# Kernel tuning notes

Measured on AMD Instinct MI355X. Metric: run time of the kernel, lower is better.

Reference implementation:

```python
import jax, jax.numpy as jnp
import numpy as np

D = 1024
H = 16
HD = 64  # head dim (bert_dim // num_heads, fixed to 64 by module)
EPS = 1e-12


def setup_inputs() -> dict:
    key = jax.random.key(0)
    ks = jax.random.split(key, 12)
    B, S1, S2 = 8, 512, 512
    scale = 0.02
    return {
        "s1_input_tensor": jax.random.normal(ks[0], (B, S1, D), jnp.float32),
        "s2_input_tensor": jax.random.normal(ks[1], (B, S2, D), jnp.float32),
        "s2_attention_mask": jnp.zeros((B, 1, 1, S2), jnp.float32),
        "Wq": jax.random.normal(ks[2], (D, D), jnp.float32) * scale,
        "bq": jnp.zeros((D,), jnp.float32),
        "Wk": jax.random.normal(ks[3], (D, D), jnp.float32) * scale,
        "bk": jnp.zeros((D,), jnp.float32),
        "Wv": jax.random.normal(ks[4], (D, D), jnp.float32) * scale,
        "bv": jnp.zeros((D,), jnp.float32),
        "Wo": jax.random.normal(ks[5], (D, D), jnp.float32) * scale,
        "bo": jnp.zeros((D,), jnp.float32),
        "ln_w": jnp.ones((D,), jnp.float32),
        "ln_b": jnp.zeros((D,), jnp.float32),
        "cl_att": 1,
    }


def _split_heads(x):
    B, S, _ = x.shape
    return x.reshape(B, S, H, HD).transpose(0, 2, 1, 3)  # [B,H,S,HD]


def _layernorm(x, w, b):
    u = jnp.mean(x, axis=-1, keepdims=True)
    s = jnp.mean(jnp.square(x - u), axis=-1, keepdims=True)
    return w * ((x - u) / jnp.sqrt(s + EPS)) + b


def reference(s1_input_tensor, s2_input_tensor, s2_attention_mask,
              Wq, bq, Wk, bk, Wv, bv, Wo, bo, ln_w, ln_b, cl_att):
    # QKV projections (dropout layers act as identity in eval)
    q = _split_heads(s1_input_tensor @ Wq + bq)   # [B,H,S1,HD]
    k = _split_heads(s2_input_tensor @ Wk + bk)   # [B,H,S2,HD]
    v = _split_heads(s2_input_tensor @ Wv + bv)   # [B,H,S2,HD]

    scores = jnp.einsum("bhqd,bhkd->bhqk", q, k) / jnp.sqrt(jnp.float32(HD))
    scores = scores + s2_attention_mask           # broadcast [B,1,1,S2]
    probs = jax.nn.softmax(scores, axis=-1)
    if cl_att:  # static Python flag: second, inverted softmax pass
        probs = jax.nn.softmax(1.0 - probs + s2_attention_mask, axis=-1)

    ctx = jnp.einsum("bhqk,bhkd->bhqd", probs, v)  # [B,H,S1,HD]
    B, _, S1, _ = ctx.shape
    ctx = ctx.transpose(0, 2, 1, 3).reshape(B, S1, D)

    # output dense + residual + LayerNorm
    h = ctx @ Wo + bo
    return _layernorm(h + s1_input_tensor, ln_w, ln_b)
```

## Files before the change

kernel.cpp:

```cpp
#include <hip/hip_runtime.h>
#include <cstdint>

#define DEV static __device__ __forceinline__

typedef __attribute__((ext_vector_type(8))) short bf16x8;
typedef __attribute__((ext_vector_type(4))) short bf16x4v;
typedef __attribute__((ext_vector_type(4))) float f32x4;
typedef __attribute__((ext_vector_type(4))) unsigned u32x4;

DEV float bf2f(short s) {
  union { unsigned u; float f; } c; c.u = ((unsigned)(unsigned short)s) << 16; return c.f;
}
DEV short f2bf(float f) {
  union { float f; unsigned u; } c; c.f = f;
  unsigned r = c.u + 0x7FFF + ((c.u >> 16) & 1);
  return (short)(r >> 16);
}
DEV unsigned cvtpk(float lo, float hi) {
  unsigned r;
  asm("v_cvt_pk_bf16_f32 %0, %1, %2" : "=v"(r) : "v"(lo), "v"(hi));
  return r;
}
DEV void g2lds16(const void* g, void* l) {
  __builtin_amdgcn_global_load_lds(
      (const __attribute__((address_space(1))) void*)g,
      (__attribute__((address_space(3))) void*)l, 16, 0, 0);
}

__global__ __launch_bounds__(256) void prep_kernel(
    const float* __restrict__ s1, short* __restrict__ s1b,
    const float* __restrict__ s2, short* __restrict__ s2b,
    const float* __restrict__ w0, short* __restrict__ t0,
    const float* __restrict__ w1, short* __restrict__ t1,
    const float* __restrict__ w2, short* __restrict__ t2,
    const float* __restrict__ w3, short* __restrict__ t3) {
  __shared__ float tile[32][33];
  const int bid = blockIdx.x, tid = threadIdx.x;
  if (bid < 8192) {
    int i = bid * 256 + tid;
    const float* in = s1; short* out = s1b;
    if (i >= 1048576) { i -= 1048576; in = s2; out = s2b; }
    float4 v = reinterpret_cast<const float4*>(in)[i];
    bf16x4v o; o[0] = f2bf(v.x); o[1] = f2bf(v.y); o[2] = f2bf(v.z); o[3] = f2bf(v.w);
    reinterpret_cast<bf16x4v*>(out)[i] = o;
  } else {
    int b2 = bid - 8192;
    int z = b2 >> 10, rem = b2 & 1023;
    int bx = rem & 31, by = rem >> 5;
    int tx = tid & 31, ty = tid >> 5;
    const float* W; short* Wt;
    switch (z) {
      case 0: W = w0; Wt = t0; break;
      case 1: W = w1; Wt = t1; break;
      case 2: W = w2; Wt = t2; break;
      default: W = w3; Wt = t3; break;
    }
#pragma unroll
    for (int j = 0; j < 4; ++j)
      tile[ty + 8 * j][tx] = W[(size_t)(by * 32 + ty + 8 * j) * 1024 + bx * 32 + tx];
    __syncthreads();
#pragma unroll
    for (int j = 0; j < 4; ++j)
      Wt[(size_t)(bx * 32 + ty + 8 * j) * 1024 + by * 32 + tx] = f2bf(tile[tx][ty + 8 * j]);
  }
}

template <typename EPI>
DEV void gemm_core128(const short* __restrict__ A, const short* __restrict__ Bt,
                      int m0, int n0, EPI epi) {
  __shared__ alignas(16) short As[128 * 64];
  __shared__ alignas(16) short Bs[128 * 64];
  const int tid = threadIdx.x, lane = tid & 63, w = tid >> 6;
  const int wm = (w >> 1) * 64, wn = (w & 1) * 64;

  f32x4 acc[4][4] = {};

  for (int kt = 0; kt < 16; ++kt) {
    __syncthreads();
#pragma unroll
    for (int rnd = 0; rnd < 4; ++rnd) {
      int c = tid + rnd * 256;
      int row = c >> 3, ch = c & 7;
      g2lds16(A + (size_t)(m0 + row) * 1024 + kt * 64 + ch * 8, (char*)As + c * 16);
    }
#pragma unroll
    for (int rnd = 0; rnd < 4; ++rnd) {
      int c = tid + rnd * 256;
      int row = c >> 3, ch = c & 7;
      g2lds16(Bt + (size_t)(n0 + row) * 1024 + kt * 64 + ch * 8, (char*)Bs + c * 16);
    }
    asm volatile("s_waitcnt vmcnt(0)" ::: "memory");
    __syncthreads();
#pragma unroll
    for (int kk = 0; kk < 64; kk += 32) {
      bf16x8 a[4], b[4];
#pragma unroll
      for (int i = 0; i < 4; ++i)
        a[i] = *reinterpret_cast<const bf16x8*>(&As[(wm + i * 16 + (lane & 15)) * 64 + kk + 8 * (lane >> 4)]);
#pragma unroll
      for (int i = 0; i < 4; ++i)
        b[i] = *reinterpret_cast<const bf16x8*>(&Bs[(wn + i * 16 + (lane & 15)) * 64 + kk + 8 * (lane >> 4)]);
#pragma unroll
      for (int mi = 0; mi < 4; ++mi)
#pragma unroll
        for (int ni = 0; ni < 4; ++ni)
          acc[mi][ni] = __builtin_amdgcn_mfma_f32_16x16x32_bf16(a[mi], b[ni], acc[mi][ni], 0, 0, 0);
    }
  }
#pragma unroll
  for (int mi = 0; mi < 4; ++mi)
#pragma unroll
    for (int ni = 0; ni < 4; ++ni)
#pragma unroll
      for (int r = 0; r < 4; ++r) {
        int m = m0 + wm + mi * 16 + 4 * (lane >> 4) + r;
        int n = n0 + wn + ni * 16 + (lane & 15);
        epi(m, n, acc[mi][ni][r]);
      }
}

__global__ __launch_bounds__(256) void qkv_gemm_kernel(
    const short* __restrict__ s1b, const short* __restrict__ s2b,
    const short* __restrict__ wqt, const short* __restrict__ wkt,
    const short* __restrict__ wvt,
    const float* __restrict__ bq, const float* __restrict__ bk,
    const float* __restrict__ bv,
    short* __restrict__ qb, short* __restrict__ kb, short* __restrict__ vtb) {
  const int z = blockIdx.z;
  int flat = blockIdx.y * 8 + blockIdx.x;
  int r8 = flat & 7, q8 = flat >> 3;
  int lg = r8 * 32 + q8;
  if (z < 2) {
    const short* A = (z == 0) ? s1b : s2b;
    const short* Bt = (z == 0) ? wqt : wkt;
    const float* bias = (z == 0) ? bq : bk;
    short* out = (z == 0) ? qb : kb;
    int n0 = (lg & 7) * 128, m0 = (lg >> 3) * 128;
    gemm_core128(A, Bt, m0, n0, [&](int m, int n, float v) {
      v += bias[n];
      out[(((size_t)(m >> 9) * 16 + (n >> 6)) * 512 + (m & 511)) * 64 + (n & 63)] = f2bf(v);
    });
  } else {
    int m0 = (lg & 7) * 128, n0 = (lg >> 3) * 128;
    gemm_core128(wvt, s2b, m0, n0, [&](int m, int n, float v) {
      v += bv[m];
      vtb[(((size_t)(n >> 9) * 16 + (m >> 6)) * 64 + (m & 63)) * 512 + (n & 511)] = f2bf(v);
    });
  }
}

__global__ __launch_bounds__(256) void wo_gemm_kernel(
    const short* __restrict__ A, const short* __restrict__ Bt,
    const float* __restrict__ bias, const float* __restrict__ s1,
    float* __restrict__ out) {
  int flat = blockIdx.y * 8 + blockIdx.x;
  int r8 = flat & 7, q8 = flat >> 3;
  int lg = r8 * 32 + q8;
  int n0 = (lg & 7) * 128, m0 = (lg >> 3) * 128;
  gemm_core128(A, Bt, m0, n0, [&](int m, int n, float v) {
    out[(size_t)m * 1024 + n] = v + bias[n] + s1[(size_t)m * 1024 + n];
  });
}

__global__ __launch_bounds__(256, 2) void attn_kernel(
    const short* __restrict__ Qg, const short* __restrict__ Kg,
    const short* __restrict__ Vtg, const float* __restrict__ maskg,
    const int* __restrict__ clp, short* __restrict__ ctx) {
  const int tid = threadIdx.x, lane = tid & 63, w = tid >> 6;
  const int l15 = lane & 15, l4 = lane >> 4;
  int flat = blockIdx.y * 8 + blockIdx.x;
  int r8 = flat & 7, q8 = flat >> 3;
  int lg = r8 * 128 + q8;
  const int qt = lg & 7, bh = lg >> 3, b = bh >> 4;
  const int cl = clp[0];
  const float* mrow = maskg + b * 512;

  const short* qbase = Qg + ((size_t)bh * 512 + qt * 64 + w * 16 + l15) * 64 + 8 * l4;
  bf16x8 qf0 = *reinterpret_cast<const bf16x8*>(qbase);
  bf16x8 qf1 = *reinterpret_cast<const bf16x8*>(qbase + 32);

  unsigned P[64];
  float m1 = -1e30f;
  const short* kbh = Kg + (size_t)bh * 512 * 64 + 8 * l4;
  const bool odd = (l4 & 1);

#pragma unroll
  for (int kt = 0; kt < 8; ++kt) {
#pragma unroll
    for (int ni = 0; ni < 4; ++ni) {
      const short* kp = kbh + (size_t)(kt * 64 + ni * 16 + l15) * 64;
      bf16x8 k0 = *reinterpret_cast<const bf16x8*>(kp);
      bf16x8 k1 = *reinterpret_cast<const bf16x8*>(kp + 32);
      f32x4 acc = {};
      acc = __builtin_amdgcn_mfma_f32_16x16x32_bf16(k0, qf0, acc, 0, 0, 0);
      acc = __builtin_amdgcn_mfma_f32_16x16x32_bf16(k1, qf1, acc, 0, 0, 0);
      f32x4 mk = *reinterpret_cast<const f32x4*>(&mrow[kt * 64 + ni * 16 + 4 * l4]);
      float s0 = fmaf(acc[0], 0.125f, mk[0]);
      float s1v = fmaf(acc[1], 0.125f, mk[1]);
      float s2v = fmaf(acc[2], 0.125f, mk[2]);
      float s3 = fmaf(acc[3], 0.125f, mk[3]);
      m1 = fmaxf(m1, fmaxf(fmaxf(s0, s1v), fmaxf(s2v, s3)));
      unsigned pk0 = cvtpk(s0, s1v), pk1 = cvtpk(s2v, s3);
      unsigned e0 = __shfl_xor(pk0, 16), e1 = __shfl_xor(pk1, 16);
      unsigned h0 = odd ? e0 : pk0;
      unsigned h1 = odd ? e1 : pk1;
      unsigned h2 = odd ? pk0 : e0;
      unsigned h3 = odd ? pk1 : e1;
      unsigned g0 = __shfl_xor(h0, 32), g1 = __shfl_xor(h1, 32);
      unsigned g2 = __shfl_xor(h2, 32), g3 = __shfl_xor(h3, 32);
      bool ist = (((l4 >> 1) & 1) == (ni & 1));
      bool useh = ((l4 & 1) == (ni & 1));
      unsigned w0 = useh ? h0 : g0;
      unsigned w1 = useh ? h1 : g1;
      unsigned w2 = useh ? h2 : g2;
      unsigned w3 = useh ? h3 : g3;
      const int mIdx = kt * 2 + (ni >> 1);
      P[4 * mIdx + 0] = ist ? w0 : P[4 * mIdx + 0];
      P[4 * mIdx + 1] = ist ? w1 : P[4 * mIdx + 1];
      P[4 * mIdx + 2] = ist ? w2 : P[4 * mIdx + 2];
      P[4 * mIdx + 3] = ist ? w3 : P[4 * mIdx + 3];
    }
  }

  m1 = fmaxf(m1, __shfl_xor(m1, 16));
  m1 = fmaxf(m1, __shfl_xor(m1, 32));
  float Z1 = 0.f;
#pragma unroll
  for (int i = 0; i < 64; ++i) {
    unsigned u = P[i];
    float lo = __uint_as_float(u << 16);
    float hi = __uint_as_float(u & 0xffff0000u);
    float e0 = __expf(lo - m1), e1 = __expf(hi - m1);
    Z1 += e0 + e1;
    P[i] = cvtpk(e0, e1);
  }
  Z1 += __shfl_xor(Z1, 16); Z1 += __shfl_xor(Z1, 32);
  float rZ1 = 1.0f / Z1;
  float rowscale = rZ1;

  if (cl) {
    float m2 = -1e30f;
#pragma unroll
    for (int m = 0; m < 16; ++m) {
      f32x4 mka = *reinterpret_cast<const f32x4*>(&mrow[32 * m + 8 * l4]);
      f32x4 mkb = *reinterpret_cast<const f32x4*>(&mrow[32 * m + 8 * l4 + 4]);
#pragma unroll
      for (int j = 0; j < 4; ++j) {
        unsigned u = P[4 * m + j];
        float p0 = __uint_as_float(u << 16) * rZ1;
        float p1 = __uint_as_float(u & 0xffff0000u) * rZ1;
        float mv0 = (j < 2) ? mka[2 * j] : mkb[2 * j - 4];
        float mv1 = (j < 2) ? mka[2 * j + 1] : mkb[2 * j - 3];
        m2 = fmaxf(m2, fmaxf(1.0f - p0 + mv0, 1.0f - p1 + mv1));
      }
    }
    m2 = fmaxf(m2, __shfl_xor(m2, 16));
    m2 = fmaxf(m2, __shfl_xor(m2, 32));
    float Z2 = 0.f;
#pragma unroll
    for (int m = 0; m < 16; ++m) {
      f32x4 mka = *reinterpret_cast<const f32x4*>(&mrow[32 * m + 8 * l4]);
      f32x4 mkb = *reinterpret_cast<const f32x4*>(&mrow[32 * m + 8 * l4 + 4]);
#pragma unroll
      for (int j = 0; j < 4; ++j) {
        unsigned u = P[4 * m + j];
        float p0 = __uint_as_float(u << 16) * rZ1;
        float p1 = __uint_as_float(u & 0xffff0000u) * rZ1;
        float mv0 = (j < 2) ? mka[2 * j] : mkb[2 * j - 4];
        float mv1 = (j < 2) ? mka[2 * j + 1] : mkb[2 * j - 3];
        float e0 = __expf(1.0f - p0 + mv0 - m2);
        float e1 = __expf(1.0f - p1 + mv1 - m2);
        Z2 += e0 + e1;
        P[4 * m + j] = cvtpk(e0, e1);
      }
    }
    Z2 += __shfl_xor(Z2, 16); Z2 += __shfl_xor(Z2, 32);
    rowscale = 1.0f / Z2;
  }

  f32x4 o[4] = {};
  const short* vbh = Vtg + (size_t)bh * 64 * 512 + 8 * l4;
#pragma unroll
  for (int m = 0; m < 16; ++m) {
    u32x4 av;
    av[0] = P[4 * m + 0]; av[1] = P[4 * m + 1];
    av[2] = P[4 * m + 2]; av[3] = P[4 * m + 3];
    bf16x8 a = __builtin_bit_cast(bf16x8, av);
    bf16x8 b0 = *reinterpret_cast<const bf16x8*>(vbh + (size_t)(0 * 16 + l15) * 512 + m * 32);
    bf16x8 b1 = *reinterpret_cast<const bf16x8*>(vbh + (size_t)(1 * 16 + l15) * 512 + m * 32);
    bf16x8 b2 = *reinterpret_cast<const bf16x8*>(vbh + (size_t)(2 * 16 + l15) * 512 + m * 32);
    bf16x8 b3 = *reinterpret_cast<const bf16x8*>(vbh + (size_t)(3 * 16 + l15) * 512 + m * 32);
    __builtin_amdgcn_s_setprio(1);
    o[0] = __builtin_amdgcn_mfma_f32_16x16x32_bf16(a, b0, o[0], 0, 0, 0);
    o[1] = __builtin_amdgcn_mfma_f32_16x16x32_bf16(a, b1, o[1], 0, 0, 0);
    o[2] = __builtin_amdgcn_mfma_f32_16x16x32_bf16(a, b2, o[2], 0, 0, 0);
    o[3] = __builtin_amdgcn_mfma_f32_16x16x32_bf16(a, b3, o[3], 0, 0, 0);
    __builtin_amdgcn_s_setprio(0);
  }
  float sc[4];
#pragma unroll
  for (int r = 0; r < 4; ++r) sc[r] = __shfl(rowscale, 4 * l4 + r);
  const int h = bh & 15;
#pragma unroll
  for (int ni = 0; ni < 4; ++ni)
#pragma unroll
    for (int r = 0; r < 4; ++r) {
      int s = qt * 64 + w * 16 + 4 * l4 + r;
      int d = ni * 16 + l15;
      ctx[((size_t)b * 512 + s) * 1024 + h * 64 + d] = f2bf(o[ni][r] * sc[r]);
    }
}

__global__ __launch_bounds__(256) void ln_kernel(
    const float* __restrict__ hbuf,
    const float* __restrict__ lw, const float* __restrict__ lb,
    float* __restrict__ out) {
  __shared__ float red[8];
  const int row = blockIdx.x, tid = threadIdx.x;
  float4 hv = reinterpret_cast<const float4*>(hbuf + (size_t)row * 1024)[tid];
  float x0 = hv.x, x1 = hv.y, x2 = hv.z, x3 = hv.w;
  float s = x0 + x1 + x2 + x3;
  float ss = x0 * x0 + x1 * x1 + x2 * x2 + x3 * x3;
  for (int o = 32; o; o >>= 1) { s += __shfl_down(s, o); ss += __shfl_down(ss, o); }
  int w = tid >> 6;
  if ((tid & 63) == 0) { red[w] = s; red[4 + w] = ss; }
  __syncthreads();
  float S = red[0] + red[1] + red[2] + red[3];
  float SS = red[4] + red[5] + red[6] + red[7];
  float u = S * (1.f / 1024.f);
  float var = SS * (1.f / 1024.f) - u * u;
  float inv = rsqrtf(var + 1e-12f);
  float4 wv = reinterpret_cast<const float4*>(lw)[tid];
  float4 bv = reinterpret_cast<const float4*>(lb)[tid];
  float4 ov;
  ov.x = wv.x * (x0 - u) * inv + bv.x;
  ov.y = wv.y * (x1 - u) * inv + bv.y;
  ov.z = wv.z * (x2 - u) * inv + bv.z;
  ov.w = wv.w * (x3 - u) * inv + bv.w;
  reinterpret_cast<float4*>(out + (size_t)row * 1024)[tid] = ov;
}

extern "C" void kernel_launch(void* const* d_in, const int* in_sizes, int n_in,
                              void* d_out, int out_size, void* d_ws, size_t ws_size,
                              hipStream_t stream) {
  const float* s1 = (const float*)d_in[0];
  const float* s2 = (const float*)d_in[1];
  const float* mask = (const float*)d_in[2];
  const float* Wq = (const float*)d_in[3]; const float* bq = (const float*)d_in[4];
  const float* Wk = (const float*)d_in[5]; const float* bk = (const float*)d_in[6];
  const float* Wv = (const float*)d_in[7]; const float* bv = (const float*)d_in[8];
  const float* Wo = (const float*)d_in[9]; const float* bo = (const float*)d_in[10];
  const float* lnw = (const float*)d_in[11]; const float* lnb = (const float*)d_in[12];
  const int* cl = (const int*)d_in[13];
  float* out = (float*)d_out;

  char* ws = (char*)d_ws;
  short* s1b = (short*)ws; ws += (size_t)4096 * 1024 * 2;
  short* s2b = (short*)ws; ws += (size_t)4096 * 1024 * 2;
  short* wqt = (short*)ws; ws += (size_t)1024 * 1024 * 2;
  short* wkt = (short*)ws; ws += (size_t)1024 * 1024 * 2;
  short* wvt = (short*)ws; ws += (size_t)1024 * 1024 * 2;
  short* wot = (short*)ws; ws += (size_t)1024 * 1024 * 2;
  short* qb  = (short*)ws; ws += (size_t)4096 * 1024 * 2;
  short* kb  = (short*)ws; ws += (size_t)4096 * 1024 * 2;
  short* vtb = (short*)ws; ws += (size_t)4096 * 1024 * 2;
  short* ctxb= (short*)ws; ws += (size_t)4096 * 1024 * 2;
  float* hb  = (float*)ws; ws += (size_t)4096 * 1024 * 4;

  prep_kernel<<<12288, 256, 0, stream>>>(s1, s1b, s2, s2b,
                                         Wq, wqt, Wk, wkt, Wv, wvt, Wo, wot);
  qkv_gemm_kernel<<<dim3(8, 32, 3), 256, 0, stream>>>(s1b, s2b, wqt, wkt, wvt,
                                                      bq, bk, bv, qb, kb, vtb);
  attn_kernel<<<dim3(8, 128), 256, 0, stream>>>(qb, kb, vtb, mask, cl, ctxb);
  wo_gemm_kernel<<<dim3(8, 32), 256, 0, stream>>>(ctxb, wot, bo, s1, hb);
  ln_kernel<<<4096, 256, 0, stream>>>(hb, lnw, lnb, out);
}
```

Baseline: 265.7 us.

## Stage K and V tiles through double-buffered swizzled LDS in attention kernel

Measured after the change: 237.2 us. 1.12x faster.

```diff
diff --git a/kernel.cpp b/kernel.cpp
--- a/kernel.cpp
+++ b/kernel.cpp
@@ -166,6 +166,8 @@
     const short* __restrict__ Qg, const short* __restrict__ Kg,
     const short* __restrict__ Vtg, const float* __restrict__ maskg,
     const int* __restrict__ clp, short* __restrict__ ctx) {
+  __shared__ alignas(16) short KV[2][64 * 64];
+
   const int tid = threadIdx.x, lane = tid & 63, w = tid >> 6;
   const int l15 = lane & 15, l4 = lane >> 4;
   int flat = blockIdx.y * 8 + blockIdx.x;
@@ -175,25 +177,55 @@
   const int cl = clp[0];
   const float* mrow = maskg + b * 512;
 
+  const char* kbh = (const char*)(Kg + (size_t)bh * 512 * 64);
+  const char* vbh = (const char*)(Vtg + (size_t)bh * 64 * 512);
+
+  auto stageK = [&](int t, int buf) {
+#pragma unroll
+    for (int rnd = 0; rnd < 2; ++rnd) {
+      int s = tid + rnd * 256;
+      int r = s >> 3, cs = s & 7;
+      g2lds16(kbh + (size_t)(t * 64 + r) * 128 + ((cs ^ (r & 7)) * 16),
+              (char*)KV[buf] + s * 16);
+    }
+  };
+  auto stageV = [&](int t, int buf) {
+#pragma unroll
+    for (int rnd = 0; rnd < 2; ++rnd) {
+      int s = tid + rnd * 256;
+      int r = s >> 3, cs = s & 7;
+      g2lds16(vbh + (size_t)r * 1024 + t * 128 + ((cs ^ (r & 7)) * 16),
+              (char*)KV[buf] + s * 16);
+    }
+  };
+  auto ldfrag = [&](const short* base, int r, int c) -> bf16x8 {
+    return *reinterpret_cast<const bf16x8*>(base + r * 64 + ((c ^ (r & 7)) * 8));
+  };
+
   const short* qbase = Qg + ((size_t)bh * 512 + qt * 64 + w * 16 + l15) * 64 + 8 * l4;
   bf16x8 qf0 = *reinterpret_cast<const bf16x8*>(qbase);
   bf16x8 qf1 = *reinterpret_cast<const bf16x8*>(qbase + 32);
 
   unsigned P[64];
   float m1 = -1e30f;
-  const short* kbh = Kg + (size_t)bh * 512 * 64 + 8 * l4;
   const bool odd = (l4 & 1);
 
+  stageK(0, 0);
+  asm volatile("s_waitcnt vmcnt(0)" ::: "memory");
+  __syncthreads();
 #pragma unroll
   for (int kt = 0; kt < 8; ++kt) {
+    if (kt + 1 < 8) stageK(kt + 1, (kt + 1) & 1);
+    const short* kb = KV[kt & 1];
 #pragma unroll
     for (int ni = 0; ni < 4; ++ni) {
-      const short* kp = kbh + (size_t)(kt * 64 + ni * 16 + l15) * 64;
-      bf16x8 k0 = *reinterpret_cast<const bf16x8*>(kp);
-      bf16x8 k1 = *reinterpret_cast<const bf16x8*>(kp + 32);
+      bf16x8 k0 = ldfrag(kb, ni * 16 + l15, l4);
+      bf16x8 k1 = ldfrag(kb, ni * 16 + l15, 4 + l4);
       f32x4 acc = {};
+      __builtin_amdgcn_s_setprio(1);
       acc = __builtin_amdgcn_mfma_f32_16x16x32_bf16(k0, qf0, acc, 0, 0, 0);
       acc = __builtin_amdgcn_mfma_f32_16x16x32_bf16(k1, qf1, acc, 0, 0, 0);
+      __builtin_amdgcn_s_setprio(0);
       f32x4 mk = *reinterpret_cast<const f32x4*>(&mrow[kt * 64 + ni * 16 + 4 * l4]);
       float s0 = fmaf(acc[0], 0.125f, mk[0]);
       float s1v = fmaf(acc[1], 0.125f, mk[1]);
@@ -220,7 +252,13 @@
       P[4 * mIdx + 2] = ist ? w2 : P[4 * mIdx + 2];
       P[4 * mIdx + 3] = ist ? w3 : P[4 * mIdx + 3];
     }
-  }
+    if (kt + 1 < 8) {
+      asm volatile("s_waitcnt vmcnt(0)" ::: "memory");
+      __syncthreads();
+    }
+  }
+
+  stageV(0, 0);
 
   m1 = fmaxf(m1, __shfl_xor(m1, 16));
   m1 = fmaxf(m1, __shfl_xor(m1, 32));
@@ -278,24 +316,35 @@
     rowscale = 1.0f / Z2;
   }
 
+  asm volatile("s_waitcnt vmcnt(0)" ::: "memory");
+  __syncthreads();
   f32x4 o[4] = {};
-  const short* vbh = Vtg + (size_t)bh * 64 * 512 + 8 * l4;
-#pragma unroll
-  for (int m = 0; m < 16; ++m) {
-    u32x4 av;
-    av[0] = P[4 * m + 0]; av[1] = P[4 * m + 1];
-    av[2] = P[4 * m + 2]; av[3] = P[4 * m + 3];
-    bf16x8 a = __builtin_bit_cast(bf16x8, av);
-    bf16x8 b0 = *reinterpret_cast<const bf16x8*>(vbh + (size_t)(0 * 16 + l15) * 512 + m * 32);
-    bf16x8 b1 = *reinterpret_cast<const bf16x8*>(vbh + (size_t)(1 * 16 + l15) * 512 + m * 32);
-    bf16x8 b2 = *reinterpret_cast<const bf16x8*>(vbh + (size_t)(2 * 16 + l15) * 512 + m * 32);
-    bf16x8 b3 = *reinterpret_cast<const bf16x8*>(vbh + (size_t)(3 * 16 + l15) * 512 + m * 32);
-    __builtin_amdgcn_s_setprio(1);
-    o[0] = __builtin_amdgcn_mfma_f32_16x16x32_bf16(a, b0, o[0], 0, 0, 0);
-    o[1] = __builtin_amdgcn_mfma_f32_16x16x32_bf16(a, b1, o[1], 0, 0, 0);
-    o[2] = __builtin_amdgcn_mfma_f32_16x16x32_bf16(a, b2, o[2], 0, 0, 0);
-    o[3] = __builtin_amdgcn_mfma_f32_16x16x32_bf16(a, b3, o[3], 0, 0, 0);
-    __builtin_amdgcn_s_setprio(0);
+#pragma unroll
+  for (int t = 0; t < 8; ++t) {
+    if (t + 1 < 8) stageV(t + 1, (t + 1) & 1);
+    const short* vb = KV[t & 1];
+#pragma unroll
+    for (int kk = 0; kk < 2; ++kk) {
+      const int m = t * 2 + kk;
+      u32x4 av;
+      av[0] = P[4 * m + 0]; av[1] = P[4 * m + 1];
+      av[2] = P[4 * m + 2]; av[3] = P[4 * m + 3];
+      bf16x8 a = __builtin_bit_cast(bf16x8, av);
+      bf16x8 b0 = ldfrag(vb, 0 * 16 + l15, kk * 4 + l4);
+      bf16x8 b1 = ldfrag(vb, 1 * 16 + l15, kk * 4 + l4);
+      bf16x8 b2 = ldfrag(vb, 2 * 16 + l15, kk * 4 + l4);
+      bf16x8 b3 = ldfrag(vb, 3 * 16 + l15, kk * 4 + l4);
+      __builtin_amdgcn_s_setprio(1);
+      o[0] = __builtin_amdgcn_mfma_f32_16x16x32_bf16(a, b0, o[0], 0, 0, 0);
+      o[1] = __builtin_amdgcn_mfma_f32_16x16x32_bf16(a, b1, o[1], 0, 0, 0);
+      o[2] = __builtin_amdgcn_mfma_f32_16x16x32_bf16(a, b2, o[2], 0, 0, 0);
+      o[3] = __builtin_amdgcn_mfma_f32_16x16x32_bf16(a, b3, o[3], 0, 0, 0);
+      __builtin_amdgcn_s_setprio(0);
+    }
+    if (t + 1 < 8) {
+      asm volatile("s_waitcnt vmcnt(0)" ::: "memory");
+      __syncthreads();
+    }
   }
   float sc[4];
 #pragma unroll
```
